# Kernel tuning notes

Hardware: AMD Instinct MI355X
Metric: run time of the kernel (lower is better)

Reference implementation:

```python
import jax, jax.numpy as jnp
import numpy as np

B, S, D, H = 8, 1024, 768, 12
DH = D // H  # per-head dim = 64


def setup_inputs() -> dict:
    key = jax.random.key(0)
    ks = jax.random.split(key, 9)
    scale = 1.0 / np.sqrt(D)
    x = jax.random.normal(ks[0], (B, S, D), dtype=jnp.float32)
    # Per-head projection weights stacked over the head axis [H, D, DH]
    Wq = jax.random.normal(ks[1], (H, D, DH), dtype=jnp.float32) * scale
    bq = jax.random.normal(ks[2], (H, DH), dtype=jnp.float32) * 0.02
    Wk = jax.random.normal(ks[3], (H, D, DH), dtype=jnp.float32) * scale
    bk = jax.random.normal(ks[4], (H, DH), dtype=jnp.float32) * 0.02
    Wv = jax.random.normal(ks[5], (H, D, DH), dtype=jnp.float32) * scale
    bv = jax.random.normal(ks[6], (H, DH), dtype=jnp.float32) * 0.02
    Wo = jax.random.normal(ks[7], (D, D), dtype=jnp.float32) * scale
    bo = jax.random.normal(ks[8], (D,), dtype=jnp.float32) * 0.02
    return {"x": x, "Wq": Wq, "bq": bq, "Wk": Wk, "bk": bk,
            "Wv": Wv, "bv": bv, "Wo": Wo, "bo": bo}


def reference(x, Wq, bq, Wk, bk, Wv, bv, Wo, bo):
    # Batched equivalent of the per-head Python loop: each head has its own
    # Q/K/V linear projections (weights stacked on the head axis).
    q = jnp.einsum('bsd,hde->bhse', x, Wq) + bq[None, :, None, :]
    k = jnp.einsum('bsd,hde->bhse', x, Wk) + bk[None, :, None, :]
    v = jnp.einsum('bsd,hde->bhse', x, Wv) + bv[None, :, None, :]
    scores = jnp.einsum('bhse,bhte->bhst', q, k) / jnp.sqrt(jnp.float32(DH))
    attn = jax.nn.softmax(scores, axis=-1)
    out = jnp.einsum('bhst,bhte->bhse', attn, v)  # [B,H,S,DH]
    # concat heads on last dim -> [B,S,H*DH] = [B,S,D]
    out = out.transpose(0, 2, 1, 3).reshape(B, S, D)
    return out @ Wo.T + bo
```

## Files before the change

### kernel.cpp

```cpp
#include <hip/hip_runtime.h>
#include <hip/hip_bf16.h>


typedef unsigned short u16;
typedef unsigned int u32;
typedef __attribute__((ext_vector_type(8))) short bf16x8;
typedef __attribute__((ext_vector_type(8))) unsigned short u16x8;
typedef __attribute__((ext_vector_type(4))) float f32x4;
typedef __attribute__((ext_vector_type(4))) u32 u32x4;

typedef __attribute__((address_space(1))) const u32* gas_u32;
typedef __attribute__((address_space(3))) u32* las_u32;

#define DEVI __device__ __forceinline__

DEVI u16 f2bf(float f) {
  union { float f; u32 u; } v; v.f = f;
  u32 r = v.u + 0x7fffu + ((v.u >> 16) & 1u);
  return (u16)(r >> 16);
}

DEVI void gll16(const void* g, void* l) {
  __builtin_amdgcn_global_load_lds((gas_u32)g, (las_u32)l, 16, 0, 0);
}

DEVI f32x4 mfma16(bf16x8 a, bf16x8 b, f32x4 c) {
  return __builtin_amdgcn_mfma_f32_16x16x32_bf16(a, b, c, 0, 0, 0);
}

DEVI u32 cvtpk(float lo, float hi) {
  u32 r;
  asm("v_cvt_pk_bf16_f32 %0, %1, %2" : "=v"(r) : "v"(lo), "v"(hi));
  return r;
}

__global__ __launch_bounds__(256) void k_prep(const float* __restrict__ x,
                                              u16* __restrict__ xb,
                                              const float* __restrict__ Wo,
                                              u16* __restrict__ Wob,
                                              const float* __restrict__ Wq,
                                              const float* __restrict__ Wk,
                                              const float* __restrict__ Wv,
                                              u16* __restrict__ Wtb) {
  __shared__ u16 T[64][65];
  const int blk = blockIdx.x;
  const int tid = threadIdx.x;
  if (blk < 6720) {
    const float* in; u16* out; int idx;
    if (blk < 6144) { in = x;  out = xb;  idx = blk * 256 + tid; }
    else            { in = Wo; out = Wob; idx = (blk - 6144) * 256 + tid; }
    float4 v = ((const float4*)in)[idx];
    ushort4 o;
    o.x = f2bf(v.x); o.y = f2bf(v.y); o.z = f2bf(v.z); o.w = f2bf(v.w);
    ((ushort4*)out)[idx] = o;
    return;
  }
  const int blk2 = blk - 6720;
  const int th = blk2 / 12;
  const int k0 = (blk2 % 12) * 64;
  const float* W = (th < 12) ? Wq : (th < 24) ? Wk : Wv;
  const int h = th % 12;
  W += (size_t)h * 768 * 64;
  const int row = tid >> 2, c = tid & 3;
  const float* src = W + (size_t)(k0 + row) * 64 + c * 16;
#pragma unroll
  for (int j = 0; j < 4; ++j) {
    float4 v = ((const float4*)src)[j];
    T[row][c * 16 + j * 4 + 0] = f2bf(v.x);
    T[row][c * 16 + j * 4 + 1] = f2bf(v.y);
    T[row][c * 16 + j * 4 + 2] = f2bf(v.z);
    T[row][c * 16 + j * 4 + 3] = f2bf(v.w);
  }
  __syncthreads();
  const int e = tid >> 2;
  u16* dst = Wtb + ((size_t)th * 64 + e) * 768 + k0 + c * 16;
  alignas(16) u16 tmp[16];
#pragma unroll
  for (int j = 0; j < 16; ++j) tmp[j] = T[c * 16 + j][e];
  *(u16x8*)(dst)     = *(const u16x8*)(tmp);
  *(u16x8*)(dst + 8) = *(const u16x8*)(tmp + 8);
}

__global__ __launch_bounds__(256, 3) void k_gemmQKV(const u16* __restrict__ Ab,
                                                    const u16* __restrict__ Wtb,
                                                    const float* __restrict__ bq,
                                                    const float* __restrict__ bk,
                                                    const float* __restrict__ bv,
                                                    u16* __restrict__ Qb,
                                                    u16* __restrict__ VTb) {
  __shared__ u16 smem[20480];
  const int tid = threadIdx.x;
  const int w = tid >> 6, lane = tid & 63, lq = lane & 15, g = lane >> 4;
  const int wm = w >> 1, wn = w & 1;
  const int m0 = blockIdx.x * 128;
  const int ph = blockIdx.y;
  const u16* Arows = Ab + (size_t)m0 * 768;
  const u16* B0 = Wtb + (size_t)ph * 64 * 768;
  const u16* B1 = Wtb + (size_t)(12 + ph) * 64 * 768;
  const u16* B2 = Wtb + (size_t)(24 + ph) * 64 * 768;

  f32x4 acc[3][4][2];
#pragma unroll
  for (int s = 0; s < 3; ++s)
#pragma unroll
    for (int mf = 0; mf < 4; ++mf)
#pragma unroll
      for (int nf = 0; nf < 2; ++nf) acc[s][mf][nf] = (f32x4){0.f, 0.f, 0.f, 0.f};

  for (int kt = 0; kt < 12; ++kt) {
    const int kb = kt * 64;
#pragma unroll
    for (int i = 0; i < 4; ++i) {
      int c = w * 4 + i;
      int id = c * 64 + lane;
      int row = id >> 3, cb = id & 7;
      gll16(Arows + (size_t)row * 768 + kb + ((cb ^ (row & 7)) << 3), &smem[c * 512]);
    }
#pragma unroll
    for (int i = 0; i < 2; ++i) {
      int c = w * 2 + i;
      int id = c * 64 + lane;
      int row = id >> 3, cb = id & 7;
      int sw = (cb ^ (row & 7)) << 3;
      size_t off = (size_t)row * 768 + kb + sw;
      gll16(B0 + off, &smem[8192 + c * 512]);
      gll16(B1 + off, &smem[12288 + c * 512]);
      gll16(B2 + off, &smem[16384 + c * 512]);
    }
    asm volatile("s_waitcnt vmcnt(0)" ::: "memory");
    __syncthreads();
#pragma unroll
    for (int kk = 0; kk < 2; ++kk) {
      bf16x8 a[4];
#pragma unroll
      for (int mf = 0; mf < 4; ++mf) {
        int row = wm * 64 + mf * 16 + lq;
        a[mf] = *(const bf16x8*)(&smem[0] + row * 64 +
                                 (((kk * 64 + g * 16) ^ ((row & 7) << 4)) >> 1));
      }
#pragma unroll
      for (int s = 0; s < 3; ++s) {
        bf16x8 b[2];
#pragma unroll
        for (int nf = 0; nf < 2; ++nf) {
          int row = wn * 32 + nf * 16 + lq;
          b[nf] = *(const bf16x8*)(&smem[8192 + s * 4096] + row * 64 +
                                   (((kk * 64 + g * 16) ^ ((row & 7) << 4)) >> 1));
        }
#pragma unroll
        for (int mf = 0; mf < 4; ++mf)
#pragma unroll
          for (int nf = 0; nf < 2; ++nf)
            acc[s][mf][nf] = mfma16(a[mf], b[nf], acc[s][mf][nf]);
      }
    }
    if (kt < 11) __syncthreads();
  }

  const int b = m0 >> 10;
#pragma unroll
  for (int s = 0; s < 2; ++s) {
    u16* out = Qb + (size_t)s * 6291456;
    const float qs = s ? 1.0f : 0.18033688f;
    const float* bp = s ? bk : bq;
#pragma unroll
    for (int nf = 0; nf < 2; ++nf) {
      const int e = wn * 32 + nf * 16 + lq;
      const float bi = bp[ph * 64 + e];
#pragma unroll
      for (int mf = 0; mf < 4; ++mf)
#pragma unroll
        for (int r = 0; r < 4; ++r) {
          int srow = (m0 & 1023) + wm * 64 + mf * 16 + 4 * g + r;
          out[((size_t)(b * 12 + ph) * 1024 + srow) * 64 + e] =
              f2bf((acc[s][mf][nf][r] + bi) * qs);
        }
    }
  }
  __syncthreads();
  u16* Ct = &smem[0];
#pragma unroll
  for (int nf = 0; nf < 2; ++nf) {
    const int e = wn * 32 + nf * 16 + lq;
    const float bi = bv[ph * 64 + e];
#pragma unroll
    for (int mf = 0; mf < 4; ++mf)
#pragma unroll
      for (int r = 0; r < 4; ++r) {
        int sl = wm * 64 + mf * 16 + 4 * g + r;
        Ct[e * 136 + sl] = f2bf(acc[2][mf][nf][r] + bi);
      }
  }
  __syncthreads();
  const int er = tid >> 2, cc = tid & 3;
  u16* dst = VTb + ((size_t)(b * 12 + ph) * 64 + er) * 1024 + (m0 & 1023) + cc * 32;
#pragma unroll
  for (int i = 0; i < 4; ++i)
    *(u16x8*)(dst + i * 8) = *(const u16x8*)(Ct + er * 136 + cc * 32 + i * 8);
}

__global__ __launch_bounds__(256) void k_gemmO(const u16* __restrict__ Ab,
                                               const u16* __restrict__ Bb,
                                               const float* __restrict__ bias,
                                               float* __restrict__ out) {
  __shared__ u16 smem[2][12288];
  const int tid = threadIdx.x;
  const int w = tid >> 6, lane = tid & 63, lq = lane & 15, g = lane >> 4;
  const int wm = w >> 1, wn = w & 1;
  const int m0 = blockIdx.x * 128;
  const int pn = blockIdx.y;
  const u16* Arows = Ab + (size_t)m0 * 768;
  const u16* Brows = Bb + (size_t)pn * 64 * 768;

  f32x4 acc[4][2];
#pragma unroll
  for (int mf = 0; mf < 4; ++mf)
#pragma unroll
    for (int nf = 0; nf < 2; ++nf) acc[mf][nf] = (f32x4){0.f, 0.f, 0.f, 0.f};

#define OSTAGE(buf, kt_)                                                         \
  {                                                                              \
    const int kb_ = (kt_) * 64;                                                  \
    _Pragma("unroll")                                                            \
    for (int i = 0; i < 4; ++i) {                                                \
      int c = w * 4 + i;                                                         \
      int id = c * 64 + lane;                                                    \
      int row = id >> 3, cb = id & 7;                                            \
      gll16(Arows + (size_t)row * 768 + kb_ + ((cb ^ (row & 7)) << 3),           \
            &smem[buf][c * 512]);                                                \
    }                                                                            \
    _Pragma("unroll")                                                            \
    for (int i = 0; i < 2; ++i) {                                                \
      int c = w * 2 + i;                                                         \
      int id = c * 64 + lane;                                                    \
      int row = id >> 3, cb = id & 7;                                            \
      gll16(Brows + (size_t)row * 768 + kb_ + ((cb ^ (row & 7)) << 3),           \
            &smem[buf][8192 + c * 512]);                                         \
    }                                                                            \
  }

#define OCOMP(buf)                                                               \
  {                                                                              \
    const u16* As_ = &smem[buf][0];                                              \
    const u16* Bs_ = &smem[buf][8192];                                           \
    _Pragma("unroll")                                                            \
    for (int kk = 0; kk < 2; ++kk) {                                             \
      bf16x8 a[4], b[2];                                                         \
      _Pragma("unroll")                                                          \
      for (int mf = 0; mf < 4; ++mf) {                                           \
        int row = wm * 64 + mf * 16 + lq;                                        \
        a[mf] = *(const bf16x8*)(As_ + row * 64 +                                \
                                 (((kk * 64 + g * 16) ^ ((row & 7) << 4)) >> 1)); \
      }                                                                          \
      _Pragma("unroll")                                                          \
      for (int nf = 0; nf < 2; ++nf) {                                           \
        int row = wn * 32 + nf * 16 + lq;                                        \
        b[nf] = *(const bf16x8*)(Bs_ + row * 64 +                                \
                                 (((kk * 64 + g * 16) ^ ((row & 7) << 4)) >> 1)); \
      }                                                                          \
      _Pragma("unroll")                                                          \
      for (int mf = 0; mf < 4; ++mf)                                             \
        _Pragma("unroll")                                                        \
        for (int nf = 0; nf < 2; ++nf)                                           \
          acc[mf][nf] = mfma16(a[mf], b[nf], acc[mf][nf]);                       \
    }                                                                            \
  }

  OSTAGE(0, 0)
  asm volatile("s_waitcnt vmcnt(0)" ::: "memory");
  __syncthreads();
  for (int it = 0; it < 6; ++it) {
    const int kt = it * 2;
    OSTAGE(1, kt + 1)
    OCOMP(0)
    asm volatile("s_waitcnt vmcnt(0)" ::: "memory");
    __syncthreads();
    if (it < 5) OSTAGE(0, kt + 2)
    OCOMP(1)
    if (it < 5) {
      asm volatile("s_waitcnt vmcnt(0)" ::: "memory");
      __syncthreads();
    }
  }
#undef OSTAGE
#undef OCOMP

#pragma unroll
  for (int nf = 0; nf < 2; ++nf) {
    const int n = pn * 64 + wn * 32 + nf * 16 + lq;
    const float bi = bias[n];
#pragma unroll
    for (int mf = 0; mf < 4; ++mf)
#pragma unroll
      for (int r = 0; r < 4; ++r) {
        int m = m0 + wm * 64 + mf * 16 + 4 * g + r;
        out[(size_t)m * 768 + n] = acc[mf][nf][r] + bi;
      }
  }
}

__global__ __launch_bounds__(512) void k_attn(const u16* __restrict__ Qb,
                                              const u16* __restrict__ Kb,
                                              const u16* __restrict__ VTb,
                                              u16* __restrict__ AO) {
  __shared__ u16 Ksm[3][4096];
  __shared__ u16 Vsm[3][4096];
  const int tid = threadIdx.x;
  const int w = tid >> 6, lane = tid & 63, lq = lane & 15, g = lane >> 4;
  const int bh = blockIdx.x, b = bh / 12, h = bh % 12;
  const int q0 = blockIdx.y * 128 + w * 16;
  const u16* Qw = Qb + ((size_t)bh * 1024 + q0) * 64;
  const u16* Kp = Kb + (size_t)bh * 65536;
  const u16* Vp = VTb + (size_t)bh * 65536;
  const bool gsel = (g & 1);

  bf16x8 qf[2];
#pragma unroll
  for (int kk = 0; kk < 2; ++kk)
    qf[kk] = *(const bf16x8*)(Qw + lq * 64 + kk * 32 + g * 8);

  f32x4 o[4];
#pragma unroll
  for (int ef = 0; ef < 4; ++ef) o[ef] = (f32x4){0.f, 0.f, 0.f, 0.f};
  float l_ = 0.f;

#define STAGE(buf, kt_)                                                          \
  {                                                                              \
    const int kb_ = (kt_) * 64;                                                  \
    const int id = w * 64 + lane;                                                \
    const int row = id >> 3, cb = id & 7;                                        \
    const int sb = cb ^ (row & 7);                                               \
    const int tb = (sb & 4) | ((sb & 1) << 1) | ((sb >> 1) & 1);                 \
    gll16(Kp + (size_t)(kb_ + row) * 64 + (sb << 3), &Ksm[buf][w * 512]);        \
    gll16(Vp + (size_t)row * 1024 + kb_ + (tb << 3), &Vsm[buf][w * 512]);        \
  }

#define TILE(buf)                                                                \
  {                                                                              \
    f32x4 s[4];                                                                  \
    _Pragma("unroll")                                                            \
    for (int kf = 0; kf < 4; ++kf) s[kf] = (f32x4){0.f, 0.f, 0.f, 0.f};          \
    __builtin_amdgcn_s_setprio(1);                                               \
    _Pragma("unroll")                                                            \
    for (int kf = 0; kf < 4; ++kf) {                                             \
      const int row = kf * 16 + lq;                                              \
      _Pragma("unroll")                                                          \
      for (int kk = 0; kk < 2; ++kk) {                                           \
        bf16x8 kfr = *(const bf16x8*)(&Ksm[buf][0] + row * 64 +                  \
                                      (((kk * 64 + g * 16) ^ ((row & 7) << 4)) >> 1)); \
        s[kf] = mfma16(kfr, qf[kk], s[kf]);                                      \
      }                                                                          \
    }                                                                            \
    __builtin_amdgcn_s_setprio(0);                                               \
    float sm = 0.f;                                                              \
    _Pragma("unroll")                                                            \
    for (int kf = 0; kf < 4; ++kf)                                               \
      _Pragma("unroll")                                                          \
      for (int r = 0; r < 4; ++r) {                                              \
        float p = __builtin_amdgcn_exp2f(s[kf][r]);                              \
        s[kf][r] = p;                                                            \
        sm += p;                                                                 \
      }                                                                          \
    l_ += sm;                                                                    \
    u32 D[4][2];                                                                 \
    _Pragma("unroll")                                                            \
    for (int kf = 0; kf < 4; ++kf) {                                             \
      D[kf][0] = cvtpk(s[kf][0], s[kf][1]);                                      \
      D[kf][1] = cvtpk(s[kf][2], s[kf][3]);                                      \
    }                                                                            \
    _Pragma("unroll")                                                            \
    for (int kk = 0; kk < 2; ++kk) {                                             \
      const int kk2 = kk * 2;                                                    \
      u32 sa0 = gsel ? D[kk2][0] : D[kk2 + 1][0];                                \
      u32 sa1 = gsel ? D[kk2][1] : D[kk2 + 1][1];                                \
      u32 xa0 = __shfl_xor(sa0, 16), xa1 = __shfl_xor(sa1, 16);                  \
      u32x4 t = { gsel ? xa0 : D[kk2][0],                                        \
                  gsel ? xa1 : D[kk2][1],                                        \
                  gsel ? D[kk2 + 1][0] : xa0,                                    \
                  gsel ? D[kk2 + 1][1] : xa1 };                                  \
      bf16x8 pb = __builtin_bit_cast(bf16x8, t);                                 \
      __builtin_amdgcn_s_setprio(1);                                             \
      _Pragma("unroll")                                                          \
      for (int ef = 0; ef < 4; ++ef) {                                           \
        const int row = ef * 16 + lq;                                            \
        bf16x8 vf = *(const bf16x8*)(&Vsm[buf][0] + row * 64 +                   \
                                     (((kk * 64 + g * 16) ^ ((row & 7) << 4)) >> 1)); \
        o[ef] = mfma16(vf, pb, o[ef]);                                           \
      }                                                                          \
      __builtin_amdgcn_s_setprio(0);                                             \
    }                                                                            \
  }

#define WAITBAR(n)                                                               \
  asm volatile("s_waitcnt vmcnt(" #n ")" ::: "memory");                          \
  __syncthreads();

  STAGE(0, 0)
  STAGE(1, 1)

  for (int it = 0; it < 4; ++it) {
    const int t3 = it * 3;
    WAITBAR(2) TILE(0) STAGE(2, t3 + 2)
    WAITBAR(2) TILE(1) STAGE(0, t3 + 3)
    WAITBAR(2) TILE(2) STAGE(1, t3 + 4)
  }
  WAITBAR(2) TILE(0) STAGE(2, 14)
  WAITBAR(2) TILE(1) STAGE(0, 15)
  WAITBAR(2) TILE(2)
  WAITBAR(0) TILE(0)

  l_ += __shfl_xor(l_, 16);
  l_ += __shfl_xor(l_, 32);

  const float inv = 1.0f / l_;
  u16* dst = AO + ((size_t)(b * 1024 + q0 + lq)) * 768 + h * 64 + g * 4;
#pragma unroll
  for (int ef = 0; ef < 4; ++ef) {
    ushort4 t;
    t.x = f2bf(o[ef][0] * inv);
    t.y = f2bf(o[ef][1] * inv);
    t.z = f2bf(o[ef][2] * inv);
    t.w = f2bf(o[ef][3] * inv);
    *(ushort4*)(dst + ef * 16) = t;
  }
#undef STAGE
#undef TILE
#undef WAITBAR
}

extern "C" void kernel_launch(void* const* d_in, const int* in_sizes, int n_in,
                              void* d_out, int out_size, void* d_ws, size_t ws_size,
                              hipStream_t stream) {
  (void)in_sizes; (void)n_in; (void)out_size; (void)ws_size;
  const float* x  = (const float*)d_in[0];
  const float* Wq = (const float*)d_in[1];
  const float* bq = (const float*)d_in[2];
  const float* Wk = (const float*)d_in[3];
  const float* bk = (const float*)d_in[4];
  const float* Wv = (const float*)d_in[5];
  const float* bv = (const float*)d_in[6];
  const float* Wo = (const float*)d_in[7];
  const float* bo = (const float*)d_in[8];

  char* ws = (char*)d_ws;
  u16* xb  = (u16*)(ws);
  u16* Wtb = (u16*)(ws + 12582912);
  u16* Wob = (u16*)(ws + 12582912 + 3538944);
  u16* Qb  = (u16*)(ws + 12582912 + 3538944 + 1179648);
  u16* Kb  = Qb + (size_t)96 * 1024 * 64;
  u16* VTb = Kb + (size_t)96 * 1024 * 64;
  u16* AO  = xb;

  k_prep<<<7152, 256, 0, stream>>>(x, xb, Wo, Wob, Wq, Wk, Wv, Wtb);

  k_gemmQKV<<<dim3(64, 12), 256, 0, stream>>>(xb, Wtb, bq, bk, bv, Qb, VTb);

  k_attn<<<dim3(96, 8), 512, 0, stream>>>(Qb, Kb, VTb, AO);

  k_gemmO<<<dim3(64, 12), 256, 0, stream>>>(AO, Wob, bo, (float*)d_out);
}
```

Measured before the change: 100.2 us.

## Software-pipeline QK^T of next tile with softmax/PV of current tile

Splits the attention tile into a QK^T stage and a softmax+PV stage, and overlaps them across tiles using two score register sets: the QK^T MFMAs for tile t+1 are issued alongside the exp and PV work for tile t. The wait before each barrier becomes vmcnt(0) with loads issued right after it, and a min-blocks hint of 6 is added to launch_bounds. The goal is to hide exp/convert/shuffle latency behind matrix work. The extra registers for the second score buffer and the occupancy hint may cause spills, and the full vmcnt drain reduces load lookahead.

```diff
diff --git a/kernel.cpp b/kernel.cpp
--- a/kernel.cpp
+++ b/kernel.cpp
@@ -299,10 +299,10 @@
   }
 }
 
-__global__ __launch_bounds__(512) void k_attn(const u16* __restrict__ Qb,
-                                              const u16* __restrict__ Kb,
-                                              const u16* __restrict__ VTb,
-                                              u16* __restrict__ AO) {
+__global__ __launch_bounds__(512, 6) void k_attn(const u16* __restrict__ Qb,
+                                                 const u16* __restrict__ Kb,
+                                                 const u16* __restrict__ VTb,
+                                                 u16* __restrict__ AO) {
   __shared__ u16 Ksm[3][4096];
   __shared__ u16 Vsm[3][4096];
   const int tid = threadIdx.x;
@@ -323,6 +323,7 @@
 #pragma unroll
   for (int ef = 0; ef < 4; ++ef) o[ef] = (f32x4){0.f, 0.f, 0.f, 0.f};
   float l_ = 0.f;
+  f32x4 sA[4], sB[4];
 
 #define STAGE(buf, kt_)                                                          \
   {                                                                              \
@@ -335,11 +336,10 @@
     gll16(Vp + (size_t)row * 1024 + kb_ + (tb << 3), &Vsm[buf][w * 512]);        \
   }
 
-#define TILE(buf)                                                                \
+#define QKT(buf, S)                                                              \
   {                                                                              \
-    f32x4 s[4];                                                                  \
-    _Pragma("unroll")                                                            \
-    for (int kf = 0; kf < 4; ++kf) s[kf] = (f32x4){0.f, 0.f, 0.f, 0.f};          \
+    _Pragma("unroll")                                                            \
+    for (int kf = 0; kf < 4; ++kf) S[kf] = (f32x4){0.f, 0.f, 0.f, 0.f};          \
     __builtin_amdgcn_s_setprio(1);                                               \
     _Pragma("unroll")                                                            \
     for (int kf = 0; kf < 4; ++kf) {                                             \
@@ -348,25 +348,29 @@
       for (int kk = 0; kk < 2; ++kk) {                                           \
         bf16x8 kfr = *(const bf16x8*)(&Ksm[buf][0] + row * 64 +                  \
                                       (((kk * 64 + g * 16) ^ ((row & 7) << 4)) >> 1)); \
-        s[kf] = mfma16(kfr, qf[kk], s[kf]);                                      \
+        S[kf] = mfma16(kfr, qf[kk], S[kf]);                                      \
       }                                                                          \
     }                                                                            \
     __builtin_amdgcn_s_setprio(0);                                               \
+  }
+
+#define SMPV(buf, S)                                                             \
+  {                                                                              \
     float sm = 0.f;                                                              \
     _Pragma("unroll")                                                            \
     for (int kf = 0; kf < 4; ++kf)                                               \
       _Pragma("unroll")                                                          \
       for (int r = 0; r < 4; ++r) {                                              \
-        float p = __builtin_amdgcn_exp2f(s[kf][r]);                              \
-        s[kf][r] = p;                                                            \
+        float p = __builtin_amdgcn_exp2f(S[kf][r]);                              \
+        S[kf][r] = p;                                                            \
         sm += p;                                                                 \
       }                                                                          \
     l_ += sm;                                                                    \
     u32 D[4][2];                                                                 \
     _Pragma("unroll")                                                            \
     for (int kf = 0; kf < 4; ++kf) {                                             \
-      D[kf][0] = cvtpk(s[kf][0], s[kf][1]);                                      \
-      D[kf][1] = cvtpk(s[kf][2], s[kf][3]);                                      \
+      D[kf][0] = cvtpk(S[kf][0], S[kf][1]);                                      \
+      D[kf][1] = cvtpk(S[kf][2], S[kf][3]);                                      \
     }                                                                            \
     _Pragma("unroll")                                                            \
     for (int kk = 0; kk < 2; ++kk) {                                             \
@@ -391,23 +395,29 @@
     }                                                                            \
   }
 
-#define WAITBAR(n)                                                               \
-  asm volatile("s_waitcnt vmcnt(" #n ")" ::: "memory");                          \
+#define WB                                                                       \
+  asm volatile("s_waitcnt vmcnt(0)" ::: "memory");                               \
   __syncthreads();
 
   STAGE(0, 0)
   STAGE(1, 1)
-
-  for (int it = 0; it < 4; ++it) {
-    const int t3 = it * 3;
-    WAITBAR(2) TILE(0) STAGE(2, t3 + 2)
-    WAITBAR(2) TILE(1) STAGE(0, t3 + 3)
-    WAITBAR(2) TILE(2) STAGE(1, t3 + 4)
-  }
-  WAITBAR(2) TILE(0) STAGE(2, 14)
-  WAITBAR(2) TILE(1) STAGE(0, 15)
-  WAITBAR(2) TILE(2)
-  WAITBAR(0) TILE(0)
+  asm volatile("s_waitcnt vmcnt(2)" ::: "memory");
+  __syncthreads();
+  QKT(0, sA)
+
+  for (int j = 0; j < 2; ++j) {
+    const int t6 = j * 6;
+    WB STAGE(2, t6 + 2) QKT(1, sB) SMPV(0, sA)
+    WB STAGE(0, t6 + 3) QKT(2, sA) SMPV(1, sB)
+    WB STAGE(1, t6 + 4) QKT(0, sB) SMPV(2, sA)
+    WB STAGE(2, t6 + 5) QKT(1, sA) SMPV(0, sB)
+    WB STAGE(0, t6 + 6) QKT(2, sB) SMPV(1, sA)
+    WB STAGE(1, t6 + 7) QKT(0, sA) SMPV(2, sB)
+  }
+  WB STAGE(2, 14) QKT(1, sB) SMPV(0, sA)
+  WB STAGE(0, 15) QKT(2, sA) SMPV(1, sB)
+  WB QKT(0, sB) SMPV(2, sA)
+  SMPV(0, sB)
 
   l_ += __shfl_xor(l_, 16);
   l_ += __shfl_xor(l_, 32);
@@ -424,8 +434,9 @@
     *(ushort4*)(dst + ef * 16) = t;
   }
 #undef STAGE
-#undef TILE
-#undef WAITBAR
+#undef QKT
+#undef SMPV
+#undef WB
 }
 
 extern "C" void kernel_launch(void* const* d_in, const int* in_sizes, int n_in,
```

Measured after the change: 178.7 us. +78.2%, slower.
